# Kernel tuning notes

Hardware: AMD Instinct MI355X
Metric: run time of the kernel (lower is better)

Reference implementation:

```python
import jax, jax.numpy as jnp
import numpy as np

BS, N, H, F_IN, F_OUT = 4, 2048, 2, 768, 768
NEG_SLOPE = 0.2

def setup_inputs() -> dict:
    key = jax.random.key(0)
    k_h, k_adj, k_w, k_as, k_ad = jax.random.split(key, 5)
    h = jax.random.normal(k_h, (BS, N, F_IN), dtype=jnp.float32)
    adj = jax.random.randint(k_adj, (BS, N, N), 0, 2) > 0  # bool adjacency
    # xavier_uniform fan_in/fan_out per torch semantics on [H, f_in, f_out]
    limit_w = float(np.sqrt(6.0 / (F_IN + F_OUT)))
    w = jax.random.uniform(k_w, (H, F_IN, F_OUT), minval=-limit_w, maxval=limit_w, dtype=jnp.float32)
    limit_a = float(np.sqrt(6.0 / (F_OUT + 1)))
    a_src = jax.random.uniform(k_as, (H, F_OUT, 1), minval=-limit_a, maxval=limit_a, dtype=jnp.float32)
    a_dst = jax.random.uniform(k_ad, (H, F_OUT, 1), minval=-limit_a, maxval=limit_a, dtype=jnp.float32)
    bias = jnp.zeros((F_OUT,), dtype=jnp.float32)
    return {"h": h, "adj": adj, "w": w, "a_src": a_src, "a_dst": a_dst, "bias": bias}

def reference(h, adj, w, a_src, a_dst, bias):
    # h: [b, n, f_in]; w: [H, f_in, f_out] -> h_prime: [b, H, n, f_out]
    h_prime = jnp.einsum('bnf,hfo->bhno', h, w)
    t = jnp.tanh(h_prime)
    attn_src = jnp.einsum('bhno,ho->bhn', t, a_src[..., 0])  # [b, H, n]
    attn_dst = jnp.einsum('bhno,ho->bhn', t, a_dst[..., 0])  # [b, H, n]
    # broadcast add: scores[b,h,i,j] = src[i] + dst[j]
    attn = attn_src[:, :, :, None] + attn_dst[:, :, None, :]
    attn = jnp.where(attn >= 0, attn, NEG_SLOPE * attn)  # leaky_relu
    n = adj.shape[-1]
    keep = adj[:, None, :, :] | jnp.eye(n, dtype=bool)[None, None]  # [b,1,n,n]
    attn = jnp.where(keep, attn, -jnp.inf)
    attn = jax.nn.softmax(attn, axis=-1)
    # dropout is identity at inference
    out = jnp.einsum('bhij,bhjo->bhio', attn, h_prime)
    return out + bias
```

## Files before the change

### kernel.cpp

```cpp
#include <hip/hip_runtime.h>
#include <hip/hip_bf16.h>
#include <cstdint>
#include <cstddef>

#define BS   4
#define NN   2048
#define NH   2
#define FIN  768
#define FOUT 768
#define NEG_SLOPE 0.2f

typedef __attribute__((ext_vector_type(8))) short short8;
typedef __attribute__((ext_vector_type(4))) float float4v;

static __device__ __forceinline__ float bits2f(unsigned short u) {
    union { unsigned int i; float f; } v; v.i = ((unsigned int)u) << 16; return v.f;
}
static __device__ __forceinline__ unsigned short f2bits(float f) {
    union { float f; unsigned int i; } v; v.f = f;
    unsigned int x = v.i;
    unsigned int r = x + 0x7fffu + ((x >> 16) & 1u);
    return (unsigned short)(r >> 16);
}
static __device__ __forceinline__ float fast_tanh(float x) {
    float xc = fminf(fmaxf(x, -20.f), 20.f);
    float e = __expf(2.f * xc);
    return (e - 1.f) / (e + 1.f);
}
static __device__ __forceinline__ void async_copy16(void* lds, const void* g) {
    __builtin_amdgcn_global_load_lds(
        (const __attribute__((address_space(1))) unsigned int*)g,
        (__attribute__((address_space(3))) unsigned int*)lds, 16, 0, 0);
}

static __device__ __forceinline__ bool detect_isf32(const unsigned short* h_raw) {
    unsigned short u = h_raw[threadIdx.x & 63];
    int e = (u >> 7) & 0xFF;
    unsigned long long m = __ballot(e >= 118 && e <= 134);
    return __popcll(m) < 48;
}
static __device__ __forceinline__ bool detect_adj8(const unsigned char* adj_raw) {
    int l = threadIdx.x & 63;
    unsigned char v = (unsigned char)(adj_raw[l * 4 + 1] | adj_raw[l * 4 + 2] |
                                      adj_raw[l * 4 + 3]);
    unsigned long long m = __ballot(v != 0);
    return __popcll(m) > 8;
}

#define NB_H   3072
#define NB_W   1152
#define NB_Z   128
__global__ __launch_bounds__(256) void k_prep(
    const void* __restrict__ hr, unsigned short* __restrict__ h_bf,
    const void* __restrict__ wr, unsigned short* __restrict__ wt_b,
    const void* __restrict__ as_raw, const void* __restrict__ ad_raw,
    const void* __restrict__ b_raw,
    float* __restrict__ asf, float* __restrict__ adf, float* __restrict__ bff,
    float* __restrict__ attn_acc)
{
    __shared__ float tile[32][33];
    int bi = blockIdx.x;
    int t = threadIdx.x;
    if (bi < NB_H) {
        bool isf = detect_isf32((const unsigned short*)hr);
        int base = (bi * 256 + t) * 8;
        if (isf) {
            float4 f0 = *((const float4*)((const float*)hr + base));
            float4 f1 = *((const float4*)((const float*)hr + base + 4));
            unsigned short v[8] = { f2bits(f0.x), f2bits(f0.y), f2bits(f0.z), f2bits(f0.w),
                                    f2bits(f1.x), f2bits(f1.y), f2bits(f1.z), f2bits(f1.w) };
            *(uint4*)(h_bf + base) = *(const uint4*)v;
        } else {
            *(uint4*)(h_bf + base) = *(const uint4*)((const unsigned short*)hr + base);
        }
        return;
    }
    if (bi < NB_H + NB_W) {
        bool isf = detect_isf32((const unsigned short*)hr);
        int wb = bi - NB_H;
        int h  = wb / 576;
        int rem = wb % 576;
        int f0 = (rem % 24) * 32;
        int o0 = (rem / 24) * 32;
        int tx = t & 31, ty = t >> 5;
        #pragma unroll
        for (int r = 0; r < 4; ++r) {
            int fl = ty * 4 + r;
            size_t idx = (size_t)h * FIN * FOUT + (size_t)(f0 + fl) * FOUT + (o0 + tx);
            tile[fl][tx] = isf ? ((const float*)wr)[idx]
                               : bits2f(((const unsigned short*)wr)[idx]);
        }
        __syncthreads();
        #pragma unroll
        for (int r = 0; r < 4; ++r) {
            int ol = ty * 4 + r;
            size_t oidx = (size_t)h * FOUT * FIN + (size_t)(o0 + ol) * FIN + (f0 + tx);
            wt_b[oidx] = f2bits(tile[tx][ol]);
        }
        return;
    }
    if (bi < NB_H + NB_W + NB_Z) {
        attn_acc[(bi - NB_H - NB_W) * 256 + t] = 0.f;
        return;
    }
    bool isf = detect_isf32((const unsigned short*)hr);
    for (int i = t; i < NH * FOUT; i += 256) {
        asf[i] = isf ? ((const float*)as_raw)[i] : bits2f(((const unsigned short*)as_raw)[i]);
        adf[i] = isf ? ((const float*)ad_raw)[i] : bits2f(((const unsigned short*)ad_raw)[i]);
    }
    for (int i = t; i < FOUT; i += 256)
        bff[i] = isf ? ((const float*)b_raw)[i] : bits2f(((const unsigned short*)b_raw)[i]);
}

#define BM 128
#define BN 128
#define BK 64
#define NXB (NN / BM)
#define NYB (FOUT / BN)
#define BLKS_PER_BATCH (NXB * NYB)
#define GEMM_GRID (BLKS_PER_BATCH * BS * NH)

__global__ __launch_bounds__(256) void k_gemm_hw(
    const unsigned short* __restrict__ hh,
    const unsigned short* __restrict__ wh,
    unsigned short* __restrict__ hpT,
    const float* __restrict__ asf, const float* __restrict__ adf,
    float* __restrict__ attn_src, float* __restrict__ attn_dst)
{
    int lid = blockIdx.x;
    int ib  = lid & 7;
    int rem = lid >> 3;
    int i0  = (rem & 15) * BM;
    int o0  = (rem >> 4) * BN;
    int b  = ib / NH, hd = ib % NH;
    const unsigned short* A  = hh + (size_t)b  * NN * FIN;
    const unsigned short* Bt = wh + (size_t)hd * FOUT * FIN;
    unsigned short*       C  = hpT + (size_t)ib * FOUT * NN;

    __shared__ __align__(16) unsigned short As[BM * BK];
    __shared__ __align__(16) unsigned short Bs[BN * BK];

    int t = threadIdx.x;
    int lane = t & 63, wave = t >> 6;
    int wm = (wave & 1) * 64, wn = (wave >> 1) * 64;
    int lm = lane & 15, quad = lane >> 4;
    int rr = lane >> 3;
    int cc = lane & 7;
    int gc = cc ^ rr;
    int e  = lm & 7;

    float4v acc[4][4] = {};

    for (int k0 = 0; k0 < FIN; k0 += BK) {
        __syncthreads();
        #pragma unroll
        for (int p = 0; p < 4; ++p) {
            int r0 = wave * 32 + p * 8;
            async_copy16(&As[r0 * BK], A  + (size_t)(i0 + r0 + rr) * FIN + k0 + gc * 8);
            async_copy16(&Bs[r0 * BK], Bt + (size_t)(o0 + r0 + rr) * FIN + k0 + gc * 8);
        }
        __syncthreads();
        #pragma unroll
        for (int kk = 0; kk < 2; ++kk) {
            int slot = ((kk << 2) | quad) ^ e;
            short8 fa[4], fb[4];
            #pragma unroll
            for (int mt = 0; mt < 4; ++mt)
                fa[mt] = *(const short8*)&As[(wm + mt * 16 + lm) * BK + slot * 8];
            #pragma unroll
            for (int nt = 0; nt < 4; ++nt)
                fb[nt] = *(const short8*)&Bs[(wn + nt * 16 + lm) * BK + slot * 8];
            #pragma unroll
            for (int mt = 0; mt < 4; ++mt)
                #pragma unroll
                for (int nt = 0; nt < 4; ++nt)
                    acc[mt][nt] = __builtin_amdgcn_mfma_f32_16x16x32_bf16(
                        fa[mt], fb[nt], acc[mt][nt], 0, 0, 0);
        }
    }

    float asv[4], adv[4];
    #pragma unroll
    for (int nt = 0; nt < 4; ++nt) {
        int o = o0 + wn + nt * 16 + lm;
        asv[nt] = asf[hd * FOUT + o];
        adv[nt] = adf[hd * FOUT + o];
    }
    #pragma unroll
    for (int mt = 0; mt < 4; ++mt) {
        float ps[4] = {0.f, 0.f, 0.f, 0.f};
        float pd[4] = {0.f, 0.f, 0.f, 0.f};
        #pragma unroll
        for (int nt = 0; nt < 4; ++nt) {
            int node = i0 + wm + mt * 16 + quad * 4;
            int o    = o0 + wn + nt * 16 + lm;
            ushort4 v;
            v.x = f2bits(acc[mt][nt][0]);
            v.y = f2bits(acc[mt][nt][1]);
            v.z = f2bits(acc[mt][nt][2]);
            v.w = f2bits(acc[mt][nt][3]);
            *(ushort4*)&C[(size_t)o * NN + node] = v;
            #pragma unroll
            for (int r = 0; r < 4; ++r) {
                float tv = fast_tanh(acc[mt][nt][r]);
                ps[r] += tv * asv[nt];
                pd[r] += tv * adv[nt];
            }
        }
        #pragma unroll
        for (int r = 0; r < 4; ++r) {
            float s = ps[r], d = pd[r];
            #pragma unroll
            for (int off = 1; off <= 8; off <<= 1) {
                s += __shfl_xor(s, off);
                d += __shfl_xor(d, off);
            }
            if (lm == 0) {
                int node = i0 + wm + mt * 16 + quad * 4 + r;
                atomicAdd(&attn_src[ib * NN + node], s);
                atomicAdd(&attn_dst[ib * NN + node], d);
            }
        }
    }
}

__global__ __launch_bounds__(256) void k_softmax_p(
    const float* __restrict__ attn_src, const float* __restrict__ attn_dst,
    const void* __restrict__ adj_raw,
    unsigned short* __restrict__ P)
{
    int blk = blockIdx.x;
    int i = blk & (NN - 1);
    int b = blk >> 11;
    bool is8 = detect_adj8((const unsigned char*)adj_raw);
    int t = threadIdx.x;
    int lane = t & 63, wave = t >> 6;
    int j0 = t * 8;

    bool keep[8];
    if (is8) {
        const unsigned char* arow = (const unsigned char*)adj_raw + ((size_t)b * NN + i) * NN;
        uint2 v = *(const uint2*)(arow + j0);
        #pragma unroll
        for (int r = 0; r < 8; ++r) {
            unsigned int w = (r < 4) ? v.x : v.y;
            keep[r] = ((w >> ((r & 3) * 8)) & 0xFFu) != 0;
        }
    } else {
        const int* arow = (const int*)adj_raw + ((size_t)b * NN + i) * NN;
        int4 v0 = *(const int4*)(arow + j0);
        int4 v1 = *(const int4*)(arow + j0 + 4);
        keep[0] = v0.x != 0; keep[1] = v0.y != 0; keep[2] = v0.z != 0; keep[3] = v0.w != 0;
        keep[4] = v1.x != 0; keep[5] = v1.y != 0; keep[6] = v1.z != 0; keep[7] = v1.w != 0;
    }
    #pragma unroll
    for (int r = 0; r < 8; ++r) keep[r] = keep[r] || (j0 + r == i);

    __shared__ float redm[NH][4], reds[NH][4];
    int bh0 = b * NH;
    float src0 = attn_src[(size_t)bh0 * NN + i];
    float src1 = attn_src[(size_t)(bh0 + 1) * NN + i];
    const float* drow0 = attn_dst + (size_t)bh0 * NN;
    const float* drow1 = attn_dst + (size_t)(bh0 + 1) * NN;
    float4 a0 = *(const float4*)(drow0 + j0);
    float4 a1 = *(const float4*)(drow0 + j0 + 4);
    float4 c0 = *(const float4*)(drow1 + j0);
    float4 c1 = *(const float4*)(drow1 + j0 + 4);
    float dj0[8] = { a0.x, a0.y, a0.z, a0.w, a1.x, a1.y, a1.z, a1.w };
    float dj1[8] = { c0.x, c0.y, c0.z, c0.w, c1.x, c1.y, c1.z, c1.w };

    float s0[8], s1[8];
    float lm0 = -1e30f, lm1 = -1e30f;
    #pragma unroll
    for (int r = 0; r < 8; ++r) {
        float sc0 = src0 + dj0[r];
        sc0 = sc0 >= 0.f ? sc0 : NEG_SLOPE * sc0;
        s0[r] = keep[r] ? sc0 : -1e30f;
        lm0 = fmaxf(lm0, s0[r]);
        float sc1 = src1 + dj1[r];
        sc1 = sc1 >= 0.f ? sc1 : NEG_SLOPE * sc1;
        s1[r] = keep[r] ? sc1 : -1e30f;
        lm1 = fmaxf(lm1, s1[r]);
    }
    #pragma unroll
    for (int off = 32; off > 0; off >>= 1) {
        lm0 = fmaxf(lm0, __shfl_xor(lm0, off));
        lm1 = fmaxf(lm1, __shfl_xor(lm1, off));
    }
    if (lane == 0) { redm[0][wave] = lm0; redm[1][wave] = lm1; }
    __syncthreads();
    float m0 = fmaxf(fmaxf(redm[0][0], redm[0][1]), fmaxf(redm[0][2], redm[0][3]));
    float m1 = fmaxf(fmaxf(redm[1][0], redm[1][1]), fmaxf(redm[1][2], redm[1][3]));

    float p0[8], p1[8];
    float ls0 = 0.f, ls1 = 0.f;
    #pragma unroll
    for (int r = 0; r < 8; ++r) {
        p0[r] = __expf(s0[r] - m0); ls0 += p0[r];
        p1[r] = __expf(s1[r] - m1); ls1 += p1[r];
    }
    #pragma unroll
    for (int off = 32; off > 0; off >>= 1) {
        ls0 += __shfl_xor(ls0, off);
        ls1 += __shfl_xor(ls1, off);
    }
    if (lane == 0) { reds[0][wave] = ls0; reds[1][wave] = ls1; }
    __syncthreads();
    float inv0 = 1.0f / (reds[0][0] + reds[0][1] + reds[0][2] + reds[0][3]);
    float inv1 = 1.0f / (reds[1][0] + reds[1][1] + reds[1][2] + reds[1][3]);

    uint4 pw;
    pw.x = ((unsigned int)f2bits(p0[1] * inv0) << 16) | f2bits(p0[0] * inv0);
    pw.y = ((unsigned int)f2bits(p0[3] * inv0) << 16) | f2bits(p0[2] * inv0);
    pw.z = ((unsigned int)f2bits(p0[5] * inv0) << 16) | f2bits(p0[4] * inv0);
    pw.w = ((unsigned int)f2bits(p0[7] * inv0) << 16) | f2bits(p0[6] * inv0);
    *(uint4*)&P[((size_t)bh0 * NN + i) * NN + j0] = pw;
    pw.x = ((unsigned int)f2bits(p1[1] * inv1) << 16) | f2bits(p1[0] * inv1);
    pw.y = ((unsigned int)f2bits(p1[3] * inv1) << 16) | f2bits(p1[2] * inv1);
    pw.z = ((unsigned int)f2bits(p1[5] * inv1) << 16) | f2bits(p1[4] * inv1);
    pw.w = ((unsigned int)f2bits(p1[7] * inv1) << 16) | f2bits(p1[6] * inv1);
    *(uint4*)&P[((size_t)(bh0 + 1) * NN + i) * NN + j0] = pw;
}

#define BM2 256
#define BN2 192
#define BK2 64
#define NT2 (NN / BK2)
#define GRID2 (8 * (NN / BM2) * (FOUT / BN2))

__global__ __launch_bounds__(512, 2) void k_gemm_out(
    const unsigned short* __restrict__ P,
    const unsigned short* __restrict__ hpT,
    const float* __restrict__ bf,
    void* __restrict__ outp, const unsigned short* __restrict__ h_raw)
{
    bool isf = detect_isf32(h_raw);
    int lid = blockIdx.x;
    int ib  = lid & 7;
    int rem = lid >> 3;
    int i0  = (rem & 7) * BM2;
    int o0  = (rem >> 3) * BN2;
    const unsigned short* A  = P   + (size_t)ib * NN * NN;
    const unsigned short* Bt = hpT + (size_t)ib * FOUT * NN;

    __shared__ __align__(16) unsigned short As[2][BM2 * BK2];
    __shared__ __align__(16) unsigned short Bs[2][BN2 * BK2];

    int t = threadIdx.x;
    int lane = t & 63, wave = t >> 6;
    int wr = wave >> 2, wc = wave & 3;
    int wm = wr * 128, wn = wc * 48;
    int lm = lane & 15, quad = lane >> 4;
    int e  = lm & 7;
    int rr = lane >> 3, cc = lane & 7, gc = cc ^ rr;

    float4v acc[8][3] = {};

    auto stageA = [&](int nb, int q, int kt) {
        int r0 = q * 64 + wave * 8;
        async_copy16(&As[nb][r0 * BK2],
                     A + (size_t)(i0 + r0 + rr) * NN + kt * BK2 + gc * 8);
    };
    auto stageB = [&](int nb, int q, int kt) {
        int r0 = q * 64 + wave * 8;
        async_copy16(&Bs[nb][r0 * BK2],
                     Bt + (size_t)(o0 + r0 + rr) * NN + kt * BK2 + gc * 8);
    };

    stageA(0, 0, 0); stageA(0, 1, 0); stageA(0, 2, 0); stageA(0, 3, 0);
    stageB(0, 0, 0); stageB(0, 1, 0); stageB(0, 2, 0);
    asm volatile("s_waitcnt vmcnt(0)" ::: "memory");
    __builtin_amdgcn_s_barrier();

    short8 fa[2][2];
    short8 fb[3][2];

    for (int u = 0; u < NT2; ++u) {
        int cur = u & 1, nb = cur ^ 1;
        bool more = (u + 1 < NT2);
        int kt = u + 1;
        const unsigned short* Ac = As[cur];
        const unsigned short* Bc = Bs[cur];

        #pragma unroll
        for (int nt = 0; nt < 3; ++nt)
            #pragma unroll
            for (int kk = 0; kk < 2; ++kk)
                fb[nt][kk] = *(const short8*)&Bc[(wn + nt * 16 + lm) * BK2 +
                                                 ((((kk << 2) | quad) ^ e) * 8)];
        #pragma unroll
        for (int mt = 0; mt < 2; ++mt)
            #pragma unroll
            for (int kk = 0; kk < 2; ++kk)
                fa[mt][kk] = *(const short8*)&Ac[(wm + mt * 16 + lm) * BK2 +
                                                 ((((kk << 2) | quad) ^ e) * 8)];
        if (more) { stageA(nb, 0, kt); stageA(nb, 2, kt); }
        __builtin_amdgcn_s_barrier();
        asm volatile("s_waitcnt lgkmcnt(0)" ::: "memory");
        __builtin_amdgcn_s_setprio(1);
        #pragma unroll
        for (int mt = 0; mt < 2; ++mt)
            #pragma unroll
            for (int nt = 0; nt < 3; ++nt)
                #pragma unroll
                for (int kk = 0; kk < 2; ++kk)
                    acc[mt][nt] = __builtin_amdgcn_mfma_f32_16x16x32_bf16(
                        fa[mt][kk], fb[nt][kk], acc[mt][nt], 0, 0, 0);
        __builtin_amdgcn_s_setprio(0);
        __builtin_amdgcn_s_barrier();

        #pragma unroll
        for (int mt = 0; mt < 2; ++mt)
            #pragma unroll
            for (int kk = 0; kk < 2; ++kk)
                fa[mt][kk] = *(const short8*)&Ac[(wm + 32 + mt * 16 + lm) * BK2 +
                                                 ((((kk << 2) | quad) ^ e) * 8)];
        if (more) { stageB(nb, 0, kt); stageB(nb, 1, kt); }
        __builtin_amdgcn_s_barrier();
        asm volatile("s_waitcnt lgkmcnt(0)" ::: "memory");
        __builtin_amdgcn_s_setprio(1);
        #pragma unroll
        for (int mt = 0; mt < 2; ++mt)
            #pragma unroll
            for (int nt = 0; nt < 3; ++nt)
                #pragma unroll
                for (int kk = 0; kk < 2; ++kk)
                    acc[2 + mt][nt] = __builtin_amdgcn_mfma_f32_16x16x32_bf16(
                        fa[mt][kk], fb[nt][kk], acc[2 + mt][nt], 0, 0, 0);
        __builtin_amdgcn_s_setprio(0);
        if (more) asm volatile("s_waitcnt vmcnt(4)" ::: "memory");
        else      asm volatile("s_waitcnt vmcnt(0)" ::: "memory");
        __builtin_amdgcn_s_barrier();

        #pragma unroll
        for (int mt = 0; mt < 2; ++mt)
            #pragma unroll
            for (int kk = 0; kk < 2; ++kk)
                fa[mt][kk] = *(const short8*)&Ac[(wm + 64 + mt * 16 + lm) * BK2 +
                                                 ((((kk << 2) | quad) ^ e) * 8)];
        if (more) { stageB(nb, 2, kt); stageA(nb, 1, kt); }
        __builtin_amdgcn_s_barrier();
        asm volatile("s_waitcnt lgkmcnt(0)" ::: "memory");
        __builtin_amdgcn_s_setprio(1);
        #pragma unroll
        for (int mt = 0; mt < 2; ++mt)
            #pragma unroll
            for (int nt = 0; nt < 3; ++nt)
                #pragma unroll
                for (int kk = 0; kk < 2; ++kk)
                    acc[4 + mt][nt] = __builtin_amdgcn_mfma_f32_16x16x32_bf16(
                        fa[mt][kk], fb[nt][kk], acc[4 + mt][nt], 0, 0, 0);
        __builtin_amdgcn_s_setprio(0);
        __builtin_amdgcn_s_barrier();

        #pragma unroll
        for (int mt = 0; mt < 2; ++mt)
            #pragma unroll
            for (int kk = 0; kk < 2; ++kk)
                fa[mt][kk] = *(const short8*)&Ac[(wm + 96 + mt * 16 + lm) * BK2 +
                                                 ((((kk << 2) | quad) ^ e) * 8)];
        if (more) { stageA(nb, 3, kt); }
        __builtin_amdgcn_s_barrier();
        asm volatile("s_waitcnt lgkmcnt(0)" ::: "memory");
        __builtin_amdgcn_s_setprio(1);
        #pragma unroll
        for (int mt = 0; mt < 2; ++mt)
            #pragma unroll
            for (int nt = 0; nt < 3; ++nt)
                #pragma unroll
                for (int kk = 0; kk < 2; ++kk)
                    acc[6 + mt][nt] = __builtin_amdgcn_mfma_f32_16x16x32_bf16(
                        fa[mt][kk], fb[nt][kk], acc[6 + mt][nt], 0, 0, 0);
        __builtin_amdgcn_s_setprio(0);
        if (more) asm volatile("s_waitcnt vmcnt(2)" ::: "memory");
        else      asm volatile("s_waitcnt vmcnt(0)" ::: "memory");
        __builtin_amdgcn_s_barrier();
    }

    if (isf) {
        float* C = (float*)outp + (size_t)ib * NN * FOUT;
        #pragma unroll
        for (int nt = 0; nt < 3; ++nt) {
            int o = o0 + wn + nt * 16 + lm;
            float bv = bf[o];
            #pragma unroll
            for (int mt = 0; mt < 8; ++mt) {
                int i = i0 + wm + mt * 16 + quad * 4;
                #pragma unroll
                for (int r = 0; r < 4; ++r)
                    C[(size_t)(i + r) * FOUT + o] = acc[mt][nt][r] + bv;
            }
        }
    } else {
        unsigned short* C = (unsigned short*)outp + (size_t)ib * NN * FOUT;
        #pragma unroll
        for (int nt = 0; nt < 3; ++nt) {
            int o = o0 + wn + nt * 16 + lm;
            float bv = bf[o];
            #pragma unroll
            for (int mt = 0; mt < 8; ++mt) {
                int i = i0 + wm + mt * 16 + quad * 4;
                #pragma unroll
                for (int r = 0; r < 4; ++r)
                    C[(size_t)(i + r) * FOUT + o] = f2bits(acc[mt][nt][r] + bv);
            }
        }
    }
}

extern "C" void kernel_launch(void* const* d_in, const int* in_sizes, int n_in,
                              void* d_out, int out_size, void* d_ws, size_t ws_size,
                              hipStream_t stream)
{
    const void* h_raw   = d_in[0];
    const void* adj_raw = d_in[1];
    const void* w_raw   = d_in[2];
    const void* as_raw  = d_in[3];
    const void* ad_raw  = d_in[4];
    const void* b_raw   = d_in[5];

    char* ws = (char*)d_ws;
    size_t off = 0;
    unsigned short* hpT = (unsigned short*)(ws + off); off += (size_t)BS * NH * FOUT * NN * 2;
    float* asr = (float*)(ws + off);            off += (size_t)BS * NH * NN * 4;
    float* ads = (float*)(ws + off);            off += (size_t)BS * NH * NN * 4;
    size_t uoff = off;
    unsigned short* P    = (unsigned short*)(ws + uoff);
    unsigned short* h_bf = (unsigned short*)(ws + uoff); uoff += (size_t)BS * NN * FIN * 2;
    unsigned short* wt_b = (unsigned short*)(ws + uoff); uoff += (size_t)NH * FOUT * FIN * 2;
    off += (size_t)BS * NH * NN * NN * 2;
    float* asf = (float*)(ws + off);            off += (size_t)NH * FOUT * 4;
    float* adf = (float*)(ws + off);            off += (size_t)NH * FOUT * 4;
    float* bff = (float*)(ws + off);            off += 4096;

    k_prep<<<NB_H + NB_W + NB_Z + 1, 256, 0, stream>>>(
        h_raw, h_bf, w_raw, wt_b, as_raw, ad_raw, b_raw, asf, adf, bff, asr);
    k_gemm_hw<<<dim3(GEMM_GRID), 256, 0, stream>>>(
        h_bf, wt_b, hpT, asf, adf, asr, ads);
    k_softmax_p<<<dim3(BS * NN), 256, 0, stream>>>(asr, ads, adj_raw, P);
    k_gemm_out<<<dim3(GRID2), 512, 0, stream>>>(
        P, hpT, bff, d_out, (const unsigned short*)h_raw);
}
```

Measured before the change: 269.2 us.

## Triple-buffer A tiles and prefetch two K-steps ahead in output GEMM

Grows the shared-memory A buffer in the attention-times-features GEMM from two to three slots, so A tiles are fetched two K iterations ahead while B stays double-buffered one step ahead. The staging order is reshuffled: all of B is issued in the first phase and A in the middle phases. The vmcnt waits are consolidated to the end of each iteration. The explicit lgkmcnt(0) waits after the barriers are dropped, leaving the LDS-read ordering to the compiler. The aim is to hide more global-memory latency behind MFMA work, at the cost of more LDS per block and a slightly deeper prologue.

```diff
diff --git a/kernel.cpp b/kernel.cpp
--- a/kernel.cpp
+++ b/kernel.cpp
@@ -343,7 +343,7 @@
     const unsigned short* A  = P   + (size_t)ib * NN * NN;
     const unsigned short* Bt = hpT + (size_t)ib * FOUT * NN;
 
-    __shared__ __align__(16) unsigned short As[2][BM2 * BK2];
+    __shared__ __align__(16) unsigned short As[3][BM2 * BK2];
     __shared__ __align__(16) unsigned short Bs[2][BN2 * BK2];
 
     int t = threadIdx.x;
@@ -356,31 +356,34 @@
 
     float4v acc[8][3] = {};
 
-    auto stageA = [&](int nb, int q, int kt) {
+    auto stageA = [&](int slot, int q, int kt) {
         int r0 = q * 64 + wave * 8;
-        async_copy16(&As[nb][r0 * BK2],
+        async_copy16(&As[slot][r0 * BK2],
                      A + (size_t)(i0 + r0 + rr) * NN + kt * BK2 + gc * 8);
     };
-    auto stageB = [&](int nb, int q, int kt) {
+    auto stageB = [&](int slot, int q, int kt) {
         int r0 = q * 64 + wave * 8;
-        async_copy16(&Bs[nb][r0 * BK2],
+        async_copy16(&Bs[slot][r0 * BK2],
                      Bt + (size_t)(o0 + r0 + rr) * NN + kt * BK2 + gc * 8);
     };
 
     stageA(0, 0, 0); stageA(0, 1, 0); stageA(0, 2, 0); stageA(0, 3, 0);
     stageB(0, 0, 0); stageB(0, 1, 0); stageB(0, 2, 0);
-    asm volatile("s_waitcnt vmcnt(0)" ::: "memory");
+    stageA(1, 0, 1); stageA(1, 1, 1); stageA(1, 2, 1); stageA(1, 3, 1);
+    asm volatile("s_waitcnt vmcnt(4)" ::: "memory");
     __builtin_amdgcn_s_barrier();
 
     short8 fa[2][2];
     short8 fb[3][2];
 
+    int sr = 0;
     for (int u = 0; u < NT2; ++u) {
-        int cur = u & 1, nb = cur ^ 1;
-        bool more = (u + 1 < NT2);
-        int kt = u + 1;
-        const unsigned short* Ac = As[cur];
-        const unsigned short* Bc = Bs[cur];
+        int sw = sr + 2; if (sw >= 3) sw -= 3;
+        int sbw = (u + 1) & 1;
+        bool moreA = (u < NT2 - 2);
+        bool moreB = (u < NT2 - 1);
+        const unsigned short* Ac = As[sr];
+        const unsigned short* Bc = Bs[u & 1];
 
         #pragma unroll
         for (int nt = 0; nt < 3; ++nt)
@@ -394,9 +397,8 @@
             for (int kk = 0; kk < 2; ++kk)
                 fa[mt][kk] = *(const short8*)&Ac[(wm + mt * 16 + lm) * BK2 +
                                                  ((((kk << 2) | quad) ^ e) * 8)];
-        if (more) { stageA(nb, 0, kt); stageA(nb, 2, kt); }
-        __builtin_amdgcn_s_barrier();
-        asm volatile("s_waitcnt lgkmcnt(0)" ::: "memory");
+        if (moreB) { stageB(sbw, 0, u + 1); stageB(sbw, 1, u + 1); stageB(sbw, 2, u + 1); }
+        __builtin_amdgcn_s_barrier();
         __builtin_amdgcn_s_setprio(1);
         #pragma unroll
         for (int mt = 0; mt < 2; ++mt)
@@ -415,9 +417,8 @@
             for (int kk = 0; kk < 2; ++kk)
                 fa[mt][kk] = *(const short8*)&Ac[(wm + 32 + mt * 16 + lm) * BK2 +
                                                  ((((kk << 2) | quad) ^ e) * 8)];
-        if (more) { stageB(nb, 0, kt); stageB(nb, 1, kt); }
-        __builtin_amdgcn_s_barrier();
-        asm volatile("s_waitcnt lgkmcnt(0)" ::: "memory");
+        if (moreA) { stageA(sw, 0, u + 2); stageA(sw, 1, u + 2); }
+        __builtin_amdgcn_s_barrier();
         __builtin_amdgcn_s_setprio(1);
         #pragma unroll
         for (int mt = 0; mt < 2; ++mt)
@@ -428,8 +429,6 @@
                     acc[2 + mt][nt] = __builtin_amdgcn_mfma_f32_16x16x32_bf16(
                         fa[mt][kk], fb[nt][kk], acc[2 + mt][nt], 0, 0, 0);
         __builtin_amdgcn_s_setprio(0);
-        if (more) asm volatile("s_waitcnt vmcnt(4)" ::: "memory");
-        else      asm volatile("s_waitcnt vmcnt(0)" ::: "memory");
         __builtin_amdgcn_s_barrier();
 
         #pragma unroll
@@ -438,9 +437,8 @@
             for (int kk = 0; kk < 2; ++kk)
                 fa[mt][kk] = *(const short8*)&Ac[(wm + 64 + mt * 16 + lm) * BK2 +
                                                  ((((kk << 2) | quad) ^ e) * 8)];
-        if (more) { stageB(nb, 2, kt); stageA(nb, 1, kt); }
-        __builtin_amdgcn_s_barrier();
-        asm volatile("s_waitcnt lgkmcnt(0)" ::: "memory");
+        if (moreA) { stageA(sw, 2, u + 2); stageA(sw, 3, u + 2); }
+        __builtin_amdgcn_s_barrier();
         __builtin_amdgcn_s_setprio(1);
         #pragma unroll
         for (int mt = 0; mt < 2; ++mt)
@@ -459,9 +457,7 @@
             for (int kk = 0; kk < 2; ++kk)
                 fa[mt][kk] = *(const short8*)&Ac[(wm + 96 + mt * 16 + lm) * BK2 +
                                                  ((((kk << 2) | quad) ^ e) * 8)];
-        if (more) { stageA(nb, 3, kt); }
-        __builtin_amdgcn_s_barrier();
-        asm volatile("s_waitcnt lgkmcnt(0)" ::: "memory");
+        __builtin_amdgcn_s_barrier();
         __builtin_amdgcn_s_setprio(1);
         #pragma unroll
         for (int mt = 0; mt < 2; ++mt)
@@ -472,9 +468,11 @@
                     acc[6 + mt][nt] = __builtin_amdgcn_mfma_f32_16x16x32_bf16(
                         fa[mt][kk], fb[nt][kk], acc[6 + mt][nt], 0, 0, 0);
         __builtin_amdgcn_s_setprio(0);
-        if (more) asm volatile("s_waitcnt vmcnt(2)" ::: "memory");
-        else      asm volatile("s_waitcnt vmcnt(0)" ::: "memory");
-        __builtin_amdgcn_s_barrier();
+        if (moreA)      asm volatile("s_waitcnt vmcnt(4)" ::: "memory");
+        else if (moreB) asm volatile("s_waitcnt vmcnt(0)" ::: "memory");
+        __builtin_amdgcn_s_barrier();
+
+        sr = sr + 1 == 3 ? 0 : sr + 1;
     }
 
     if (isf) {
```

After: 261.7 us. -2.8%, faster.
